# Optimization experiments

Measured on AMD Instinct MI355X. Metric: run time of the kernel, lower is better.

Reference implementation:

```python
import jax, jax.numpy as jnp
import numpy as np

N_LEAVES = 8192      # perfect binary tree, depth 13
SEQ_SIZE = 4096
EMBED = 512
NUM_CLASSES = 2


def setup_inputs() -> dict:
    key = jax.random.key(0)
    ks = jax.random.split(key, 7)
    sc = lambda n: 1.0 / np.sqrt(n)
    return {
        "leaf_seq": jax.random.normal(ks[0], (N_LEAVES, SEQ_SIZE), jnp.float32),
        # nn.Linear(sequenceSize, embedSize)
        "W_emb": jax.random.normal(ks[1], (EMBED, SEQ_SIZE), jnp.float32) * sc(SEQ_SIZE),
        "b_emb": jax.random.normal(ks[2], (EMBED,), jnp.float32) * 0.01,
        # nn.Linear(2*embedSize, embedSize)
        "W_comb": jax.random.normal(ks[3], (EMBED, 2 * EMBED), jnp.float32) * sc(2 * EMBED),
        "b_comb": jax.random.normal(ks[4], (EMBED,), jnp.float32) * 0.01,
        # nn.Linear(embedSize, numClasses)
        "W_proj": jax.random.normal(ks[5], (NUM_CLASSES, EMBED), jnp.float32) * sc(EMBED),
        "b_proj": jax.random.normal(ks[6], (NUM_CLASSES,), jnp.float32) * 0.01,
    }


def reference(leaf_seq, W_emb, b_emb, W_comb, b_comb, W_proj, b_proj):
    # Depth-batched version of the recursive traverse():
    # leaves: h = relu(embedding(seq))  -- one big GEMM instead of N batch-1 calls
    h = jax.nn.relu(leaf_seq @ W_emb.T + b_emb)            # [N_LEAVES, E]
    # internal nodes: h = relu(W(cat(left, right))), one GEMM per tree level.
    # Leaves 2i and 2i+1 are siblings (in-order perfect binary tree layout),
    # matching cat((traverse(child0), traverse(child1)), dim=1).
    while h.shape[0] > 1:                                   # fixed 13 levels at trace time
        pair = jnp.concatenate([h[0::2], h[1::2]], axis=1)  # [n/2, 2E]
        h = jax.nn.relu(pair @ W_comb.T + b_comb)           # [n/2, E]
    # root only: projection(currentNode) -> nodeProbList, cat -> [1, numClasses]
    return h @ W_proj.T + b_proj
```

## Files before the change

kernel.cpp:

```cpp
#include <hip/hip_runtime.h>
#include <stdint.h>


typedef float f32x4 __attribute__((ext_vector_type(4)));
typedef short s16x8 __attribute__((ext_vector_type(8)));
typedef unsigned short u16;

__device__ __forceinline__ u16 f2bf(float f) {
    union { float f; uint32_t u; } v; v.f = f;
    return (u16)((v.u + 0x7FFFu + ((v.u >> 16) & 1u)) >> 16);
}
__device__ __forceinline__ float bf2f(u16 h) {
    union { uint32_t u; float f; } v; v.u = ((uint32_t)h) << 16;
    return v.f;
}

__global__ __launch_bounds__(256) void split_kernel(
    const float* __restrict__ x, u16* __restrict__ hi, u16* __restrict__ lo, int n4)
{
    int i = blockIdx.x * 256 + threadIdx.x;
    if (i >= n4) return;
    float4 v = ((const float4*)x)[i];
    ushort4 h, l;
    h.x = f2bf(v.x); l.x = f2bf(v.x - bf2f(h.x));
    h.y = f2bf(v.y); l.y = f2bf(v.y - bf2f(h.y));
    h.z = f2bf(v.z); l.z = f2bf(v.z - bf2f(h.z));
    h.w = f2bf(v.w); l.w = f2bf(v.w - bf2f(h.w));
    ((ushort4*)hi)[i] = h;
    ((ushort4*)lo)[i] = l;
}

template <int T, bool AFP32>
__global__ __launch_bounds__(256, 2) void gemm_split(
    const float* __restrict__ Af,
    const u16* __restrict__ Ahi_g, const u16* __restrict__ Alo_g,
    const u16* __restrict__ Bhi_g, const u16* __restrict__ Blo_g,
    const float* __restrict__ bias,
    u16* __restrict__ Chi, u16* __restrict__ Clo,
    int K)
{
    constexpr int N = 512;
    constexpr int FM = T / 32;
    constexpr int LDW = 40;
    __shared__ u16 Ah[T][LDW], Al[T][LDW], Bh[T][LDW], Bl[T][LDW];

    const int tid  = threadIdx.x;
    const int wid  = tid >> 6;
    const int lane = tid & 63;
    const int mb = blockIdx.x * T;
    const int nb = blockIdx.y * T;
    const int wm = (wid >> 1) * (T / 2);
    const int wn = (wid & 1) * (T / 2);

    bool doA, doB; int srow, skh;
    if constexpr (T == 128) {
        doA = true; doB = true; srow = tid >> 1; skh = (tid & 1) * 16;
    } else {
        doA = (tid < 128); doB = !doA;
        const int t2 = tid & 127; srow = t2 >> 1; skh = (t2 & 1) * 16;
    }
    const long a_off = (long)(mb + srow) * K + skh;
    const long b_off = (long)(nb + srow) * K + skh;

    f32x4 acc[FM][FM];
    const f32x4 zero = {0.f, 0.f, 0.f, 0.f};
#pragma unroll
    for (int i = 0; i < FM; ++i)
#pragma unroll
        for (int j = 0; j < FM; ++j) acc[i][j] = zero;

    s16x8 rah0, rah1, ral0, ral1, rbh0, rbh1, rbl0, rbl1;

    auto load_tile = [&](int k0) {
        if (doA) {
            if constexpr (AFP32) {
                const float* p = Af + a_off + k0;
                float fa[16];
                *(float4*)(fa)      = *(const float4*)(p);
                *(float4*)(fa + 4)  = *(const float4*)(p + 4);
                *(float4*)(fa + 8)  = *(const float4*)(p + 8);
                *(float4*)(fa + 12) = *(const float4*)(p + 12);
#pragma unroll
                for (int j = 0; j < 8; ++j) {
                    u16 h = f2bf(fa[j]);
                    rah0[j] = (short)h; ral0[j] = (short)f2bf(fa[j] - bf2f(h));
                }
#pragma unroll
                for (int j = 0; j < 8; ++j) {
                    u16 h = f2bf(fa[8 + j]);
                    rah1[j] = (short)h; ral1[j] = (short)f2bf(fa[8 + j] - bf2f(h));
                }
            } else {
                rah0 = *(const s16x8*)(Ahi_g + a_off + k0);
                rah1 = *(const s16x8*)(Ahi_g + a_off + k0 + 8);
                ral0 = *(const s16x8*)(Alo_g + a_off + k0);
                ral1 = *(const s16x8*)(Alo_g + a_off + k0 + 8);
            }
        }
        if (doB) {
            rbh0 = *(const s16x8*)(Bhi_g + b_off + k0);
            rbh1 = *(const s16x8*)(Bhi_g + b_off + k0 + 8);
            rbl0 = *(const s16x8*)(Blo_g + b_off + k0);
            rbl1 = *(const s16x8*)(Blo_g + b_off + k0 + 8);
        }
    };

    load_tile(0);

    for (int k0 = 0; k0 < K; k0 += 32) {
        if (doA) {
            *(s16x8*)&Ah[srow][skh]     = rah0;
            *(s16x8*)&Ah[srow][skh + 8] = rah1;
            *(s16x8*)&Al[srow][skh]     = ral0;
            *(s16x8*)&Al[srow][skh + 8] = ral1;
        }
        if (doB) {
            *(s16x8*)&Bh[srow][skh]     = rbh0;
            *(s16x8*)&Bh[srow][skh + 8] = rbh1;
            *(s16x8*)&Bl[srow][skh]     = rbl0;
            *(s16x8*)&Bl[srow][skh + 8] = rbl1;
        }
        __syncthreads();

        if (k0 + 32 < K) load_tile(k0 + 32);

        const int r0 = lane & 15;
        const int kc = (lane >> 4) * 8;
        s16x8 afh[FM], afl[FM], bfh[FM], bfl[FM];
#pragma unroll
        for (int i = 0; i < FM; ++i) {
            afh[i] = *(const s16x8*)&Ah[wm + 16 * i + r0][kc];
            afl[i] = *(const s16x8*)&Al[wm + 16 * i + r0][kc];
            bfh[i] = *(const s16x8*)&Bh[wn + 16 * i + r0][kc];
            bfl[i] = *(const s16x8*)&Bl[wn + 16 * i + r0][kc];
        }
#pragma unroll
        for (int i = 0; i < FM; ++i)
#pragma unroll
            for (int j = 0; j < FM; ++j) {
                acc[i][j] = __builtin_amdgcn_mfma_f32_16x16x32_bf16(afh[i], bfh[j], acc[i][j], 0, 0, 0);
                acc[i][j] = __builtin_amdgcn_mfma_f32_16x16x32_bf16(afl[i], bfh[j], acc[i][j], 0, 0, 0);
                acc[i][j] = __builtin_amdgcn_mfma_f32_16x16x32_bf16(afh[i], bfl[j], acc[i][j], 0, 0, 0);
            }
        __syncthreads();
    }

    float bj[FM];
#pragma unroll
    for (int j = 0; j < FM; ++j) bj[j] = bias[nb + wn + 16 * j + (lane & 15)];
#pragma unroll
    for (int i = 0; i < FM; ++i) {
        const int grow_base = mb + wm + 16 * i + ((lane >> 4) << 2);
#pragma unroll
        for (int j = 0; j < FM; ++j) {
            const int gcol = nb + wn + 16 * j + (lane & 15);
#pragma unroll
            for (int r = 0; r < 4; ++r) {
                float v = acc[i][j][r] + bj[j];
                v = fmaxf(v, 0.f);
                u16 h = f2bf(v);
                const long idx = (long)(grow_base + r) * N + gcol;
                Chi[idx] = h;
                Clo[idx] = f2bf(v - bf2f(h));
            }
        }
    }
}

__global__ __launch_bounds__(256) void tail_kernel(
    const u16* __restrict__ Hhi, const u16* __restrict__ Hlo,
    const float* __restrict__ W,
    const float* __restrict__ bias,
    u16* __restrict__ Ohi, u16* __restrict__ Olo,
    int m)
{
    const int gid = blockIdx.x * 256 + threadIdx.x;
    if (gid >= m * 512) return;
    const int row = gid >> 9, n = gid & 511;
    const u16* hh = Hhi + (long)row * 1024;
    const u16* hl = Hlo + (long)row * 1024;
    const float* w = W + (long)n * 1024;
    float s = 0.f;
    for (int k = 0; k < 1024; k += 8) {
        s16x8 vh = *(const s16x8*)(hh + k);
        s16x8 vl = *(const s16x8*)(hl + k);
        float4 w0 = *(const float4*)(w + k);
        float4 w1 = *(const float4*)(w + k + 4);
        const float* wp = &w0.x;
#pragma unroll
        for (int j = 0; j < 4; ++j)
            s = fmaf(bf2f((u16)vh[j]) + bf2f((u16)vl[j]), wp[j], s);
        const float* wq = &w1.x;
#pragma unroll
        for (int j = 0; j < 4; ++j)
            s = fmaf(bf2f((u16)vh[4 + j]) + bf2f((u16)vl[4 + j]), wq[j], s);
    }
    float v = fmaxf(s + bias[n], 0.f);
    u16 h = f2bf(v);
    Ohi[gid] = h;
    Olo[gid] = f2bf(v - bf2f(h));
}

__global__ __launch_bounds__(128) void proj_kernel(
    const u16* __restrict__ hhi, const u16* __restrict__ hlo,
    const float* __restrict__ W, const float* __restrict__ b, float* __restrict__ out)
{
    const int c    = threadIdx.x >> 6;
    const int lane = threadIdx.x & 63;
    float s = 0.f;
#pragma unroll
    for (int j = 0; j < 8; ++j) {
        const int idx = lane + 64 * j;
        s = fmaf(bf2f(hhi[idx]) + bf2f(hlo[idx]), W[c * 512 + idx], s);
    }
#pragma unroll
    for (int off = 32; off > 0; off >>= 1) s += __shfl_down(s, off);
    if (lane == 0) out[c] = s + b[c];
}

extern "C" void kernel_launch(void* const* d_in, const int* in_sizes, int n_in,
                              void* d_out, int out_size, void* d_ws, size_t ws_size,
                              hipStream_t stream)
{
    const float* leaf   = (const float*)d_in[0];
    const float* W_emb  = (const float*)d_in[1];
    const float* b_emb  = (const float*)d_in[2];
    const float* W_comb = (const float*)d_in[3];
    const float* b_comb = (const float*)d_in[4];
    const float* W_proj = (const float*)d_in[5];
    const float* b_proj = (const float*)d_in[6];
    float* out = (float*)d_out;

    u16* p = (u16*)d_ws;
    u16* WembHi  = p; p += (size_t)512 * 4096;
    u16* WembLo  = p; p += (size_t)512 * 4096;
    u16* WcombHi = p; p += (size_t)512 * 1024;
    u16* WcombLo = p; p += (size_t)512 * 1024;
    u16* h0hi = p; p += (size_t)8192 * 512;
    u16* h0lo = p; p += (size_t)8192 * 512;
    u16* h1hi = p; p += (size_t)4096 * 512;
    u16* h1lo = p; p += (size_t)4096 * 512;

    {
        int n4 = 512 * 4096 / 4;
        split_kernel<<<(n4 + 255) / 256, 256, 0, stream>>>(W_emb, WembHi, WembLo, n4);
        n4 = 512 * 1024 / 4;
        split_kernel<<<(n4 + 255) / 256, 256, 0, stream>>>(W_comb, WcombHi, WcombLo, n4);
    }

    gemm_split<128, true><<<dim3(8192 / 128, 512 / 128), 256, 0, stream>>>(
        leaf, nullptr, nullptr, WembHi, WembLo, b_emb, h0hi, h0lo, 4096);

    u16 *chi = h0hi, *clo = h0lo, *nhi = h1hi, *nlo = h1lo;
    for (int m = 4096; m >= 1024; m >>= 1) {
        gemm_split<128, false><<<dim3(m / 128, 512 / 128), 256, 0, stream>>>(
            nullptr, chi, clo, WcombHi, WcombLo, b_comb, nhi, nlo, 1024);
        u16* t;
        t = chi; chi = nhi; nhi = t;
        t = clo; clo = nlo; nlo = t;
    }
    for (int m = 512; m >= 64; m >>= 1) {
        gemm_split<64, false><<<dim3(m / 64, 512 / 64), 256, 0, stream>>>(
            nullptr, chi, clo, WcombHi, WcombLo, b_comb, nhi, nlo, 1024);
        u16* t;
        t = chi; chi = nhi; nhi = t;
        t = clo; clo = nlo; nlo = t;
    }
    for (int m = 32; m >= 1; m >>= 1) {
        tail_kernel<<<(m * 512 + 255) / 256, 256, 0, stream>>>(
            chi, clo, W_comb, b_comb, nhi, nlo, m);
        u16* t;
        t = chi; chi = nhi; nhi = t;
        t = clo; clo = nlo; nlo = t;
    }

    proj_kernel<<<1, 128, 0, stream>>>(chi, clo, W_proj, b_proj, out);
}
```

Measured before the change: 776.6 us.

## Switch split-bf16 GEMMs to 32x32x16 MFMA with 64 tiles; shared-memory tail GEMV

Replaces the 16x16x32 MFMA GEMM (128 or 64 tiles) with a single 64x64-tile kernel using 32x32x16 bf16 MFMA and two accumulators, used for every level down to m=64. The hi half of the fp32 leaf input is now truncated instead of rounded, with the residual carrying the lost bits. The tail GEMV stages the combined input row in shared memory and spreads work over a (row, 2) grid. The aim is fewer LDS reads per MFMA, better-overlapped accumulator chains, and more blocks for the large leaf GEMM, at the cost of less reuse per block from the smaller tiles.

```diff
diff --git a/kernel.cpp b/kernel.cpp
--- a/kernel.cpp
+++ b/kernel.cpp
@@ -2,11 +2,11 @@
 #include <stdint.h>
 
 
-typedef float f32x4 __attribute__((ext_vector_type(4)));
-typedef short s16x8 __attribute__((ext_vector_type(8)));
+typedef float  f32x16 __attribute__((ext_vector_type(16)));
+typedef short  s16x8  __attribute__((ext_vector_type(8)));
 typedef unsigned short u16;
 
-__device__ __forceinline__ u16 f2bf(float f) {
+__device__ __forceinline__ u16 f2bf_rne(float f) {
     union { float f; uint32_t u; } v; v.f = f;
     return (u16)((v.u + 0x7FFFu + ((v.u >> 16) & 1u)) >> 16);
 }
@@ -22,16 +22,16 @@
     if (i >= n4) return;
     float4 v = ((const float4*)x)[i];
     ushort4 h, l;
-    h.x = f2bf(v.x); l.x = f2bf(v.x - bf2f(h.x));
-    h.y = f2bf(v.y); l.y = f2bf(v.y - bf2f(h.y));
-    h.z = f2bf(v.z); l.z = f2bf(v.z - bf2f(h.z));
-    h.w = f2bf(v.w); l.w = f2bf(v.w - bf2f(h.w));
+    h.x = f2bf_rne(v.x); l.x = f2bf_rne(v.x - bf2f(h.x));
+    h.y = f2bf_rne(v.y); l.y = f2bf_rne(v.y - bf2f(h.y));
+    h.z = f2bf_rne(v.z); l.z = f2bf_rne(v.z - bf2f(h.z));
+    h.w = f2bf_rne(v.w); l.w = f2bf_rne(v.w - bf2f(h.w));
     ((ushort4*)hi)[i] = h;
     ((ushort4*)lo)[i] = l;
 }
 
-template <int T, bool AFP32>
-__global__ __launch_bounds__(256, 2) void gemm_split(
+template <bool AFP32>
+__global__ __launch_bounds__(256, 2) void gemm32(
     const float* __restrict__ Af,
     const u16* __restrict__ Ahi_g, const u16* __restrict__ Alo_g,
     const u16* __restrict__ Bhi_g, const u16* __restrict__ Blo_g,
@@ -40,165 +40,137 @@
     int K)
 {
     constexpr int N = 512;
-    constexpr int FM = T / 32;
-    constexpr int LDW = 40;
-    __shared__ u16 Ah[T][LDW], Al[T][LDW], Bh[T][LDW], Bl[T][LDW];
+    constexpr int LDW = 56;
+    __shared__ __align__(16) u16 Ah[64][LDW], Al[64][LDW], Bh[64][LDW], Bl[64][LDW];
 
     const int tid  = threadIdx.x;
     const int wid  = tid >> 6;
     const int lane = tid & 63;
-    const int mb = blockIdx.x * T;
-    const int nb = blockIdx.y * T;
-    const int wm = (wid >> 1) * (T / 2);
-    const int wn = (wid & 1) * (T / 2);
-
-    bool doA, doB; int srow, skh;
-    if constexpr (T == 128) {
-        doA = true; doB = true; srow = tid >> 1; skh = (tid & 1) * 16;
-    } else {
-        doA = (tid < 128); doB = !doA;
-        const int t2 = tid & 127; srow = t2 >> 1; skh = (t2 & 1) * 16;
-    }
-    const long a_off = (long)(mb + srow) * K + skh;
-    const long b_off = (long)(nb + srow) * K + skh;
-
-    f32x4 acc[FM][FM];
-    const f32x4 zero = {0.f, 0.f, 0.f, 0.f};
-#pragma unroll
-    for (int i = 0; i < FM; ++i)
-#pragma unroll
-        for (int j = 0; j < FM; ++j) acc[i][j] = zero;
-
-    s16x8 rah0, rah1, ral0, ral1, rbh0, rbh1, rbl0, rbl1;
+    const int mb = blockIdx.x * 64;
+    const int nb = blockIdx.y * 64;
+    const int wm = (wid >> 1) * 32;
+    const int wn = (wid & 1) * 32;
+
+    const bool isA = tid < 128;
+    const int  t2   = tid & 127;
+    const int  srow = t2 >> 1;
+    const int  skh  = (t2 & 1) * 16;
+    const long g_off = isA ? ((long)(mb + srow) * K + skh)
+                           : ((long)(nb + srow) * K + skh);
+
+    f32x16 acc = {}, acc2 = {};
+    s16x8 rh0, rh1, rl0, rl1;
 
     auto load_tile = [&](int k0) {
-        if (doA) {
-            if constexpr (AFP32) {
-                const float* p = Af + a_off + k0;
-                float fa[16];
-                *(float4*)(fa)      = *(const float4*)(p);
-                *(float4*)(fa + 4)  = *(const float4*)(p + 4);
-                *(float4*)(fa + 8)  = *(const float4*)(p + 8);
-                *(float4*)(fa + 12) = *(const float4*)(p + 12);
-#pragma unroll
-                for (int j = 0; j < 8; ++j) {
-                    u16 h = f2bf(fa[j]);
-                    rah0[j] = (short)h; ral0[j] = (short)f2bf(fa[j] - bf2f(h));
-                }
-#pragma unroll
-                for (int j = 0; j < 8; ++j) {
-                    u16 h = f2bf(fa[8 + j]);
-                    rah1[j] = (short)h; ral1[j] = (short)f2bf(fa[8 + j] - bf2f(h));
-                }
-            } else {
-                rah0 = *(const s16x8*)(Ahi_g + a_off + k0);
-                rah1 = *(const s16x8*)(Ahi_g + a_off + k0 + 8);
-                ral0 = *(const s16x8*)(Alo_g + a_off + k0);
-                ral1 = *(const s16x8*)(Alo_g + a_off + k0 + 8);
+        if (AFP32 && isA) {
+            const float* p = Af + g_off + k0;
+            float fa[16];
+            *(float4*)(fa)      = *(const float4*)(p);
+            *(float4*)(fa + 4)  = *(const float4*)(p + 4);
+            *(float4*)(fa + 8)  = *(const float4*)(p + 8);
+            *(float4*)(fa + 12) = *(const float4*)(p + 12);
+#pragma unroll
+            for (int j = 0; j < 16; ++j) {
+                union { float f; uint32_t u; } v; v.f = fa[j];
+                u16 h = (u16)(v.u >> 16);
+                union { uint32_t u; float f; } hf; hf.u = v.u & 0xFFFF0000u;
+                u16 l = f2bf_rne(fa[j] - hf.f);
+                if (j < 8) { rh0[j] = (short)h; rl0[j] = (short)l; }
+                else       { rh1[j - 8] = (short)h; rl1[j - 8] = (short)l; }
             }
-        }
-        if (doB) {
-            rbh0 = *(const s16x8*)(Bhi_g + b_off + k0);
-            rbh1 = *(const s16x8*)(Bhi_g + b_off + k0 + 8);
-            rbl0 = *(const s16x8*)(Blo_g + b_off + k0);
-            rbl1 = *(const s16x8*)(Blo_g + b_off + k0 + 8);
+        } else {
+            const u16* ph = isA ? Ahi_g : Bhi_g;
+            const u16* pl = isA ? Alo_g : Blo_g;
+            rh0 = *(const s16x8*)(ph + g_off + k0);
+            rh1 = *(const s16x8*)(ph + g_off + k0 + 8);
+            rl0 = *(const s16x8*)(pl + g_off + k0);
+            rl1 = *(const s16x8*)(pl + g_off + k0 + 8);
         }
     };
 
     load_tile(0);
 
     for (int k0 = 0; k0 < K; k0 += 32) {
-        if (doA) {
-            *(s16x8*)&Ah[srow][skh]     = rah0;
-            *(s16x8*)&Ah[srow][skh + 8] = rah1;
-            *(s16x8*)&Al[srow][skh]     = ral0;
-            *(s16x8*)&Al[srow][skh + 8] = ral1;
-        }
-        if (doB) {
-            *(s16x8*)&Bh[srow][skh]     = rbh0;
-            *(s16x8*)&Bh[srow][skh + 8] = rbh1;
-            *(s16x8*)&Bl[srow][skh]     = rbl0;
-            *(s16x8*)&Bl[srow][skh + 8] = rbl1;
+        {
+            u16 (*Ph)[LDW] = isA ? Ah : Bh;
+            u16 (*Pl)[LDW] = isA ? Al : Bl;
+            *(s16x8*)&Ph[srow][skh]     = rh0;
+            *(s16x8*)&Ph[srow][skh + 8] = rh1;
+            *(s16x8*)&Pl[srow][skh]     = rl0;
+            *(s16x8*)&Pl[srow][skh + 8] = rl1;
         }
         __syncthreads();
 
         if (k0 + 32 < K) load_tile(k0 + 32);
 
-        const int r0 = lane & 15;
-        const int kc = (lane >> 4) * 8;
-        s16x8 afh[FM], afl[FM], bfh[FM], bfl[FM];
-#pragma unroll
-        for (int i = 0; i < FM; ++i) {
-            afh[i] = *(const s16x8*)&Ah[wm + 16 * i + r0][kc];
-            afl[i] = *(const s16x8*)&Al[wm + 16 * i + r0][kc];
-            bfh[i] = *(const s16x8*)&Bh[wn + 16 * i + r0][kc];
-            bfl[i] = *(const s16x8*)&Bl[wn + 16 * i + r0][kc];
-        }
-#pragma unroll
-        for (int i = 0; i < FM; ++i)
-#pragma unroll
-            for (int j = 0; j < FM; ++j) {
-                acc[i][j] = __builtin_amdgcn_mfma_f32_16x16x32_bf16(afh[i], bfh[j], acc[i][j], 0, 0, 0);
-                acc[i][j] = __builtin_amdgcn_mfma_f32_16x16x32_bf16(afl[i], bfh[j], acc[i][j], 0, 0, 0);
-                acc[i][j] = __builtin_amdgcn_mfma_f32_16x16x32_bf16(afh[i], bfl[j], acc[i][j], 0, 0, 0);
-            }
+        const int fr  = lane & 31;
+        const int off = (lane >> 5) * 8;
+        s16x8 ah0 = *(const s16x8*)&Ah[wm + fr][off];
+        s16x8 ah1 = *(const s16x8*)&Ah[wm + fr][16 + off];
+        s16x8 al0 = *(const s16x8*)&Al[wm + fr][off];
+        s16x8 al1 = *(const s16x8*)&Al[wm + fr][16 + off];
+        s16x8 bh0 = *(const s16x8*)&Bh[wn + fr][off];
+        s16x8 bh1 = *(const s16x8*)&Bh[wn + fr][16 + off];
+        s16x8 bl0 = *(const s16x8*)&Bl[wn + fr][off];
+        s16x8 bl1 = *(const s16x8*)&Bl[wn + fr][16 + off];
+
+        acc  = __builtin_amdgcn_mfma_f32_32x32x16_bf16(ah0, bh0, acc,  0, 0, 0);
+        acc  = __builtin_amdgcn_mfma_f32_32x32x16_bf16(ah1, bh1, acc,  0, 0, 0);
+        acc  = __builtin_amdgcn_mfma_f32_32x32x16_bf16(al0, bh0, acc,  0, 0, 0);
+        acc2 = __builtin_amdgcn_mfma_f32_32x32x16_bf16(al1, bh1, acc2, 0, 0, 0);
+        acc2 = __builtin_amdgcn_mfma_f32_32x32x16_bf16(ah0, bl0, acc2, 0, 0, 0);
+        acc2 = __builtin_amdgcn_mfma_f32_32x32x16_bf16(ah1, bl1, acc2, 0, 0, 0);
         __syncthreads();
     }
 
-    float bj[FM];
-#pragma unroll
-    for (int j = 0; j < FM; ++j) bj[j] = bias[nb + wn + 16 * j + (lane & 15)];
-#pragma unroll
-    for (int i = 0; i < FM; ++i) {
-        const int grow_base = mb + wm + 16 * i + ((lane >> 4) << 2);
-#pragma unroll
-        for (int j = 0; j < FM; ++j) {
-            const int gcol = nb + wn + 16 * j + (lane & 15);
-#pragma unroll
-            for (int r = 0; r < 4; ++r) {
-                float v = acc[i][j][r] + bj[j];
-                v = fmaxf(v, 0.f);
-                u16 h = f2bf(v);
-                const long idx = (long)(grow_base + r) * N + gcol;
-                Chi[idx] = h;
-                Clo[idx] = f2bf(v - bf2f(h));
-            }
-        }
-    }
-}
-
-__global__ __launch_bounds__(256) void tail_kernel(
+    const int fc = lane & 31;
+    const float bv = bias[nb + wn + fc];
+    const long gcol = nb + wn + fc;
+#pragma unroll
+    for (int reg = 0; reg < 16; ++reg) {
+        const int row = (reg & 3) + 8 * (reg >> 2) + 4 * (lane >> 5);
+        float v = acc[reg] + acc2[reg] + bv;
+        v = fmaxf(v, 0.f);
+        u16 h = f2bf_rne(v);
+        const long idx = (long)(mb + wm + row) * N + gcol;
+        Chi[idx] = h;
+        Clo[idx] = f2bf_rne(v - bf2f(h));
+    }
+}
+
+__global__ __launch_bounds__(256) void tail_gemv(
     const u16* __restrict__ Hhi, const u16* __restrict__ Hlo,
     const float* __restrict__ W,
     const float* __restrict__ bias,
-    u16* __restrict__ Ohi, u16* __restrict__ Olo,
-    int m)
-{
-    const int gid = blockIdx.x * 256 + threadIdx.x;
-    if (gid >= m * 512) return;
-    const int row = gid >> 9, n = gid & 511;
-    const u16* hh = Hhi + (long)row * 1024;
-    const u16* hl = Hlo + (long)row * 1024;
+    u16* __restrict__ Ohi, u16* __restrict__ Olo)
+{
+    __shared__ float hrow[1024];
+    const int row = blockIdx.x;
+    const int tid = threadIdx.x;
+    const int n   = blockIdx.y * 256 + tid;
+
+    ushort4 hv = ((const ushort4*)(Hhi + (long)row * 1024))[tid];
+    ushort4 lv = ((const ushort4*)(Hlo + (long)row * 1024))[tid];
+    hrow[4 * tid + 0] = bf2f(hv.x) + bf2f(lv.x);
+    hrow[4 * tid + 1] = bf2f(hv.y) + bf2f(lv.y);
+    hrow[4 * tid + 2] = bf2f(hv.z) + bf2f(lv.z);
+    hrow[4 * tid + 3] = bf2f(hv.w) + bf2f(lv.w);
+    __syncthreads();
+
     const float* w = W + (long)n * 1024;
     float s = 0.f;
-    for (int k = 0; k < 1024; k += 8) {
-        s16x8 vh = *(const s16x8*)(hh + k);
-        s16x8 vl = *(const s16x8*)(hl + k);
-        float4 w0 = *(const float4*)(w + k);
-        float4 w1 = *(const float4*)(w + k + 4);
-        const float* wp = &w0.x;
-#pragma unroll
-        for (int j = 0; j < 4; ++j)
-            s = fmaf(bf2f((u16)vh[j]) + bf2f((u16)vl[j]), wp[j], s);
-        const float* wq = &w1.x;
-#pragma unroll
-        for (int j = 0; j < 4; ++j)
-            s = fmaf(bf2f((u16)vh[4 + j]) + bf2f((u16)vl[4 + j]), wq[j], s);
+#pragma unroll 8
+    for (int k = 0; k < 1024; k += 4) {
+        float4 wv = *(const float4*)(w + k);
+        s = fmaf(hrow[k + 0], wv.x, s);
+        s = fmaf(hrow[k + 1], wv.y, s);
+        s = fmaf(hrow[k + 2], wv.z, s);
+        s = fmaf(hrow[k + 3], wv.w, s);
     }
     float v = fmaxf(s + bias[n], 0.f);
-    u16 h = f2bf(v);
-    Ohi[gid] = h;
-    Olo[gid] = f2bf(v - bf2f(h));
+    u16 h = f2bf_rne(v);
+    Ohi[(long)row * 512 + n] = h;
+    Olo[(long)row * 512 + n] = f2bf_rne(v - bf2f(h));
 }
 
 __global__ __launch_bounds__(128) void proj_kernel(
@@ -248,31 +220,25 @@
         split_kernel<<<(n4 + 255) / 256, 256, 0, stream>>>(W_comb, WcombHi, WcombLo, n4);
     }
 
-    gemm_split<128, true><<<dim3(8192 / 128, 512 / 128), 256, 0, stream>>>(
+    gemm32<true><<<dim3(8192 / 64, 512 / 64), 256, 0, stream>>>(
         leaf, nullptr, nullptr, WembHi, WembLo, b_emb, h0hi, h0lo, 4096);
 
     u16 *chi = h0hi, *clo = h0lo, *nhi = h1hi, *nlo = h1lo;
-    for (int m = 4096; m >= 1024; m >>= 1) {
-        gemm_split<128, false><<<dim3(m / 128, 512 / 128), 256, 0, stream>>>(
+    for (int m = 4096; m >= 64; m >>= 1) {
+        gemm32<false><<<dim3(m / 64, 512 / 64), 256, 0, stream>>>(
             nullptr, chi, clo, WcombHi, WcombLo, b_comb, nhi, nlo, 1024);
         u16* t;
         t = chi; chi = nhi; nhi = t;
         t = clo; clo = nlo; nlo = t;
     }
-    for (int m = 512; m >= 64; m >>= 1) {
-        gemm_split<64, false><<<dim3(m / 64, 512 / 64), 256, 0, stream>>>(
-            nullptr, chi, clo, WcombHi, WcombLo, b_comb, nhi, nlo, 1024);
+
+    for (int m = 32; m >= 1; m >>= 1) {
+        tail_gemv<<<dim3(m, 2), 256, 0, stream>>>(
+            chi, clo, W_comb, b_comb, nhi, nlo);
         u16* t;
         t = chi; chi = nhi; nhi = t;
         t = clo; clo = nlo; nlo = t;
     }
-    for (int m = 32; m >= 1; m >>= 1) {
-        tail_kernel<<<(m * 512 + 255) / 256, 256, 0, stream>>>(
-            chi, clo, W_comb, b_comb, nhi, nlo, m);
-        u16* t;
-        t = chi; chi = nhi; nhi = t;
-        t = clo; clo = nlo; nlo = t;
-    }
 
     proj_kernel<<<1, 128, 0, stream>>>(chi, clo, W_proj, b_proj, out);
 }
```

After: 639.3 us. -17.7%, faster.
